# Performance work log

Measured on AMD Instinct MI355X. Metric: run time of the kernel, lower is better.

The kernel has to match this reference:

```python
import jax, jax.numpy as jnp
import numpy as np

N_LAYERS = 32
HIDDEN = 1024
INTER = 2816
BATCH = 256
INIT_SCALE = 0.02


def setup_inputs() -> dict:
    key = jax.random.key(0)
    k_h, k_g, k_u, k_d = jax.random.split(key, 4)
    down_std = INIT_SCALE / np.sqrt(2 * N_LAYERS)
    h = jax.random.normal(k_h, (BATCH, N_LAYERS, HIDDEN), dtype=jnp.float32)
    # torch Linear weight layout: (out_features, in_features); stack over experts
    Wg = jax.random.normal(k_g, (N_LAYERS, INTER, HIDDEN), dtype=jnp.float32) * INIT_SCALE
    Wu = jax.random.normal(k_u, (N_LAYERS, INTER, HIDDEN), dtype=jnp.float32) * INIT_SCALE
    Wd = jax.random.normal(k_d, (N_LAYERS, HIDDEN, INTER), dtype=jnp.float32) * down_std
    return {"h": h, "Wg": Wg, "Wu": Wu, "Wd": Wd}


def reference(h, Wg, Wu, Wd):
    # h: (B, N, D); Wg/Wu: (N, I, D); Wd: (N, D, I)
    gate = jnp.einsum("bnd,nid->bni", h, Wg)
    up = jnp.einsum("bnd,nid->bni", h, Wu)
    act = jax.nn.silu(gate) * up            # (B, N, I)
    out = jnp.einsum("bni,ndi->bnd", act, Wd)  # (B, N, D)
    return out
```

## Files before the change

kernel.cpp:

```cpp
#include <hip/hip_runtime.h>
#include <hip/hip_bf16.h>

#define BATCH   256
#define NLAYERS 32
#define HID     1024
#define INTER   2816
#define BK      64

typedef __attribute__((ext_vector_type(8))) short bf16x8;
typedef __attribute__((ext_vector_type(4))) float f32x4;
typedef __attribute__((ext_vector_type(4))) int   i32x4;

__device__ __forceinline__ ushort f2bf(float f) {
  union { float f; unsigned u; } v; v.f = f;
  unsigned u = v.u;
  u += 0x7FFFu + ((u >> 16) & 1u);
  return (ushort)(u >> 16);
}

__device__ __forceinline__ void cvt_store8(ushort* dst, f32x4 a, f32x4 b) {
  bf16x8 o;
  o[0] = (short)f2bf(a[0]); o[1] = (short)f2bf(a[1]);
  o[2] = (short)f2bf(a[2]); o[3] = (short)f2bf(a[3]);
  o[4] = (short)f2bf(b[0]); o[5] = (short)f2bf(b[1]);
  o[6] = (short)f2bf(b[2]); o[7] = (short)f2bf(b[3]);
  *(bf16x8*)dst = o;
}

__global__ __launch_bounds__(512) void k_gateup(
    const float* __restrict__ h, const float* __restrict__ Wg,
    const float* __restrict__ Wu, ushort* __restrict__ act) {
  const int bid   = blockIdx.x;
  const int layer = bid / (INTER / 64);
  const int itile = bid % (INTER / 64);
  const int i0    = itile * 64;
  const int tid   = threadIdx.x;
  const int lane  = tid & 63;
  const int wave  = tid >> 6;
  const int wm    = wave >> 1;
  const int wn    = wave & 1;

  __shared__ ushort lds[BATCH * BK + 2 * 64 * BK];
  ushort* Xl = lds;
  ushort* Gl = lds + BATCH * BK;
  ushort* Ul = Gl + 64 * BK;

  f32x4 ag[4][2] = {};
  f32x4 au[4][2] = {};

  int xrow[4], xkc[4], xldst[4];
  const float* xsrc[4];
#pragma unroll
  for (int r = 0; r < 4; ++r) {
    int g = tid + 512 * r;
    xrow[r] = g >> 3;
    xkc[r]  = g & 7;
    xldst[r] = xrow[r] * BK + ((xkc[r] ^ (xrow[r] & 7)) << 3);
    xsrc[r] = h + (size_t)xrow[r] * (NLAYERS * HID) + (size_t)layer * HID + xkc[r] * 8;
  }
  const int wrow = tid >> 3, wkc = tid & 7;
  const int wldst = wrow * BK + ((wkc ^ (wrow & 7)) << 3);
  const float* gsrc = Wg + (size_t)layer * INTER * HID + (size_t)(i0 + wrow) * HID + wkc * 8;
  const float* usrc = Wu + (size_t)layer * INTER * HID + (size_t)(i0 + wrow) * HID + wkc * 8;

  f32x4 rx[4][2], rg[2], ru[2];

#pragma unroll
  for (int r = 0; r < 4; ++r) { rx[r][0] = *(const f32x4*)xsrc[r]; rx[r][1] = *(const f32x4*)(xsrc[r] + 4); }
  rg[0] = *(const f32x4*)gsrc; rg[1] = *(const f32x4*)(gsrc + 4);
  ru[0] = *(const f32x4*)usrc; ru[1] = *(const f32x4*)(usrc + 4);

  const int NK = HID / BK;
  for (int k = 0; k < NK; ++k) {
    __syncthreads();
#pragma unroll
    for (int r = 0; r < 4; ++r) cvt_store8(&Xl[xldst[r]], rx[r][0], rx[r][1]);
    cvt_store8(&Gl[wldst], rg[0], rg[1]);
    cvt_store8(&Ul[wldst], ru[0], ru[1]);
    __syncthreads();

    if (k + 1 < NK) {
      int off = (k + 1) * BK;
#pragma unroll
      for (int r = 0; r < 4; ++r) {
        rx[r][0] = *(const f32x4*)(xsrc[r] + off);
        rx[r][1] = *(const f32x4*)(xsrc[r] + off + 4);
      }
      rg[0] = *(const f32x4*)(gsrc + off); rg[1] = *(const f32x4*)(gsrc + off + 4);
      ru[0] = *(const f32x4*)(usrc + off); ru[1] = *(const f32x4*)(usrc + off + 4);
    }

#pragma unroll
    for (int ks = 0; ks < 2; ++ks) {
      const int kg = ks * 4 + (lane >> 4);
      bf16x8 af[4];
#pragma unroll
      for (int m = 0; m < 4; ++m) {
        int row = wm * 64 + m * 16 + (lane & 15);
        af[m] = *(bf16x8*)&Xl[row * BK + ((kg ^ (row & 7)) << 3)];
      }
#pragma unroll
      for (int n = 0; n < 2; ++n) {
        int row = wn * 32 + n * 16 + (lane & 15);
        int u   = row * BK + ((kg ^ (row & 7)) << 3);
        bf16x8 bg = *(bf16x8*)&Gl[u];
        bf16x8 bu = *(bf16x8*)&Ul[u];
#pragma unroll
        for (int m = 0; m < 4; ++m) {
          ag[m][n] = __builtin_amdgcn_mfma_f32_16x16x32_bf16(af[m], bg, ag[m][n], 0, 0, 0);
          au[m][n] = __builtin_amdgcn_mfma_f32_16x16x32_bf16(af[m], bu, au[m][n], 0, 0, 0);
        }
      }
    }
  }

  const int c16 = lane & 15;
  const int r4  = (lane >> 4) * 4;
#pragma unroll
  for (int m = 0; m < 4; ++m)
#pragma unroll
    for (int n = 0; n < 2; ++n)
#pragma unroll
      for (int r = 0; r < 4; ++r) {
        float g = ag[m][n][r];
        float u = au[m][n][r];
        float a = (g / (1.f + __expf(-g))) * u;
        int b = wm * 64 + m * 16 + r4 + r;
        int i = i0 + wn * 32 + n * 16 + c16;
        act[((size_t)layer * BATCH + b) * INTER + i] = f2bf(a);
      }
}

__global__ __launch_bounds__(512) void k_down(
    const ushort* __restrict__ act, const float* __restrict__ Wd,
    float* __restrict__ out) {
  const int bid   = blockIdx.x;
  const int layer = bid / (HID / 64);
  const int dtile = bid % (HID / 64);
  const int d0    = dtile * 64;
  const int tid   = threadIdx.x;
  const int lane  = tid & 63;
  const int wave  = tid >> 6;
  const int wm    = wave >> 1;
  const int wn    = wave & 1;

  __shared__ ushort lds[BATCH * BK + 64 * BK];
  ushort* Al = lds;
  ushort* Wl = lds + BATCH * BK;

  f32x4 acc[4][2] = {};

  int arow[4], akc[4], aldst[4];
  const ushort* asrc[4];
#pragma unroll
  for (int r = 0; r < 4; ++r) {
    int g = tid + 512 * r;
    arow[r] = g >> 3;
    akc[r]  = g & 7;
    aldst[r] = arow[r] * BK + ((akc[r] ^ (arow[r] & 7)) << 3);
    asrc[r] = act + ((size_t)layer * BATCH + arow[r]) * INTER + akc[r] * 8;
  }
  const int wrow = tid >> 3, wkc = tid & 7;
  const int wldst = wrow * BK + ((wkc ^ (wrow & 7)) << 3);
  const float* wsrc = Wd + (size_t)layer * HID * INTER + (size_t)(d0 + wrow) * INTER + wkc * 8;

  i32x4 ra[4];
  f32x4 rw[2];

#pragma unroll
  for (int r = 0; r < 4; ++r) ra[r] = *(const i32x4*)asrc[r];
  rw[0] = *(const f32x4*)wsrc; rw[1] = *(const f32x4*)(wsrc + 4);

  const int NK = INTER / BK;
  for (int k = 0; k < NK; ++k) {
    __syncthreads();
#pragma unroll
    for (int r = 0; r < 4; ++r) *(i32x4*)&Al[aldst[r]] = ra[r];
    cvt_store8(&Wl[wldst], rw[0], rw[1]);
    __syncthreads();

    if (k + 1 < NK) {
      int off = (k + 1) * BK;
#pragma unroll
      for (int r = 0; r < 4; ++r) ra[r] = *(const i32x4*)(asrc[r] + off);
      rw[0] = *(const f32x4*)(wsrc + off); rw[1] = *(const f32x4*)(wsrc + off + 4);
    }

#pragma unroll
    for (int ks = 0; ks < 2; ++ks) {
      const int kg = ks * 4 + (lane >> 4);
      bf16x8 af[4];
#pragma unroll
      for (int m = 0; m < 4; ++m) {
        int row = wm * 64 + m * 16 + (lane & 15);
        af[m] = *(bf16x8*)&Al[row * BK + ((kg ^ (row & 7)) << 3)];
      }
#pragma unroll
      for (int n = 0; n < 2; ++n) {
        int row = wn * 32 + n * 16 + (lane & 15);
        bf16x8 bw = *(bf16x8*)&Wl[row * BK + ((kg ^ (row & 7)) << 3)];
#pragma unroll
        for (int m = 0; m < 4; ++m)
          acc[m][n] = __builtin_amdgcn_mfma_f32_16x16x32_bf16(af[m], bw, acc[m][n], 0, 0, 0);
      }
    }
  }

  const int c16 = lane & 15;
  const int r4  = (lane >> 4) * 4;
#pragma unroll
  for (int m = 0; m < 4; ++m)
#pragma unroll
    for (int n = 0; n < 2; ++n)
#pragma unroll
      for (int r = 0; r < 4; ++r) {
        int b = wm * 64 + m * 16 + r4 + r;
        int d = d0 + wn * 32 + n * 16 + c16;
        out[(size_t)b * (NLAYERS * HID) + (size_t)layer * HID + d] = acc[m][n][r];
      }
}

extern "C" void kernel_launch(void* const* d_in, const int* in_sizes, int n_in,
                              void* d_out, int out_size, void* d_ws, size_t ws_size,
                              hipStream_t stream) {
  const float* h  = (const float*)d_in[0];
  const float* Wg = (const float*)d_in[1];
  const float* Wu = (const float*)d_in[2];
  const float* Wd = (const float*)d_in[3];
  float* out  = (float*)d_out;
  ushort* act = (ushort*)d_ws;

  hipLaunchKernelGGL(k_gateup, dim3(NLAYERS * (INTER / 64)), dim3(512), 0, stream,
                     h, Wg, Wu, act);
  hipLaunchKernelGGL(k_down, dim3(NLAYERS * (HID / 64)), dim3(512), 0, stream,
                     act, Wd, out);
}
```

Measured before the change: 368.6 us.

## Retile gate/up kernel to 128x32 tiles with BK=32 and padded LDS

The gate/up kernel moves from 256-row by 64-column tiles with BK=64 and 512 threads to 128-row by 32-column tiles with BK=32 and 256 threads. It also replaces the XOR-swizzled LDS layout with a padded row stride and uses the library bf16 conversion when staging operands. This gives 4x more, smaller blocks and less LDS per block, which should raise occupancy and spread work across more CUs. In exchange, X and weight tiles are reused less, so each element of h and the weights is fetched more times, and the k loop takes twice as many barrier-separated steps.

Measured after the change: 439.6 us. 1.19x slower.

```diff
diff --git a/kernel.cpp b/kernel.cpp
--- a/kernel.cpp
+++ b/kernel.cpp
@@ -5,130 +5,130 @@
 #define NLAYERS 32
 #define HID     1024
 #define INTER   2816
-#define BK      64
 
 typedef __attribute__((ext_vector_type(8))) short bf16x8;
 typedef __attribute__((ext_vector_type(4))) float f32x4;
 typedef __attribute__((ext_vector_type(4))) int   i32x4;
 
 __device__ __forceinline__ ushort f2bf(float f) {
+  __hip_bfloat16 b = __float2bfloat16(f);
+  return *reinterpret_cast<ushort*>(&b);
+}
+
+__device__ __forceinline__ ushort f2bf_rne(float f) {
   union { float f; unsigned u; } v; v.f = f;
   unsigned u = v.u;
   u += 0x7FFFu + ((u >> 16) & 1u);
   return (ushort)(u >> 16);
 }
 
-__device__ __forceinline__ void cvt_store8(ushort* dst, f32x4 a, f32x4 b) {
-  bf16x8 o;
-  o[0] = (short)f2bf(a[0]); o[1] = (short)f2bf(a[1]);
-  o[2] = (short)f2bf(a[2]); o[3] = (short)f2bf(a[3]);
-  o[4] = (short)f2bf(b[0]); o[5] = (short)f2bf(b[1]);
-  o[6] = (short)f2bf(b[2]); o[7] = (short)f2bf(b[3]);
-  *(bf16x8*)dst = o;
-}
-
-__global__ __launch_bounds__(512) void k_gateup(
+__device__ __forceinline__ void cvt_store4(ushort* dst, f32x4 a) {
+  ushort4 o;
+  o.x = f2bf(a[0]); o.y = f2bf(a[1]); o.z = f2bf(a[2]); o.w = f2bf(a[3]);
+  *(ushort4*)dst = o;
+}
+
+#define LDR 40
+
+__global__ __launch_bounds__(256) void k_gateup(
     const float* __restrict__ h, const float* __restrict__ Wg,
     const float* __restrict__ Wu, ushort* __restrict__ act) {
   const int bid   = blockIdx.x;
-  const int layer = bid / (INTER / 64);
-  const int itile = bid % (INTER / 64);
-  const int i0    = itile * 64;
+  const int layer = bid / 176;
+  const int rem   = bid % 176;
+  const int it    = rem >> 1;
+  const int mt    = rem & 1;
+  const int i0    = it * 32;
+  const int m0    = mt * 128;
   const int tid   = threadIdx.x;
   const int lane  = tid & 63;
   const int wave  = tid >> 6;
   const int wm    = wave >> 1;
   const int wn    = wave & 1;
 
-  __shared__ ushort lds[BATCH * BK + 2 * 64 * BK];
-  ushort* Xl = lds;
-  ushort* Gl = lds + BATCH * BK;
-  ushort* Ul = Gl + 64 * BK;
-
-  f32x4 ag[4][2] = {};
-  f32x4 au[4][2] = {};
-
-  int xrow[4], xkc[4], xldst[4];
-  const float* xsrc[4];
+  __shared__ ushort Xl[128 * LDR];
+  __shared__ ushort Gl[32 * LDR];
+  __shared__ ushort Ul[32 * LDR];
+
+  f32x4 ag[4] = {}, au[4] = {};
+
+  const float* xsrc[4]; int xdst[4];
 #pragma unroll
   for (int r = 0; r < 4; ++r) {
-    int g = tid + 512 * r;
-    xrow[r] = g >> 3;
-    xkc[r]  = g & 7;
-    xldst[r] = xrow[r] * BK + ((xkc[r] ^ (xrow[r] & 7)) << 3);
-    xsrc[r] = h + (size_t)xrow[r] * (NLAYERS * HID) + (size_t)layer * HID + xkc[r] * 8;
-  }
-  const int wrow = tid >> 3, wkc = tid & 7;
-  const int wldst = wrow * BK + ((wkc ^ (wrow & 7)) << 3);
-  const float* gsrc = Wg + (size_t)layer * INTER * HID + (size_t)(i0 + wrow) * HID + wkc * 8;
-  const float* usrc = Wu + (size_t)layer * INTER * HID + (size_t)(i0 + wrow) * HID + wkc * 8;
-
-  f32x4 rx[4][2], rg[2], ru[2];
-
-#pragma unroll
-  for (int r = 0; r < 4; ++r) { rx[r][0] = *(const f32x4*)xsrc[r]; rx[r][1] = *(const f32x4*)(xsrc[r] + 4); }
-  rg[0] = *(const f32x4*)gsrc; rg[1] = *(const f32x4*)(gsrc + 4);
-  ru[0] = *(const f32x4*)usrc; ru[1] = *(const f32x4*)(usrc + 4);
-
-  const int NK = HID / BK;
+    int g = tid + 256 * r;
+    int row = g >> 3, u = g & 7;
+    xsrc[r] = h + (size_t)(m0 + row) * (NLAYERS * HID) + (size_t)layer * HID + u * 4;
+    xdst[r] = row * LDR + u * 4;
+  }
+  const int grow = tid >> 3, gu = tid & 7;
+  const int gdst = grow * LDR + gu * 4;
+  const float* gsrc = Wg + (size_t)layer * INTER * HID + (size_t)(i0 + grow) * HID + gu * 4;
+  const float* usrc = Wu + (size_t)layer * INTER * HID + (size_t)(i0 + grow) * HID + gu * 4;
+
+  f32x4 rx[4], rg, ru;
+#pragma unroll
+  for (int r = 0; r < 4; ++r) rx[r] = *(const f32x4*)xsrc[r];
+  rg = *(const f32x4*)gsrc;
+  ru = *(const f32x4*)usrc;
+
+  const int NK = HID / 32;
   for (int k = 0; k < NK; ++k) {
     __syncthreads();
 #pragma unroll
-    for (int r = 0; r < 4; ++r) cvt_store8(&Xl[xldst[r]], rx[r][0], rx[r][1]);
-    cvt_store8(&Gl[wldst], rg[0], rg[1]);
-    cvt_store8(&Ul[wldst], ru[0], ru[1]);
+    for (int r = 0; r < 4; ++r) cvt_store4(&Xl[xdst[r]], rx[r]);
+    cvt_store4(&Gl[gdst], rg);
+    cvt_store4(&Ul[gdst], ru);
     __syncthreads();
 
     if (k + 1 < NK) {
-      int off = (k + 1) * BK;
-#pragma unroll
-      for (int r = 0; r < 4; ++r) {
-        rx[r][0] = *(const f32x4*)(xsrc[r] + off);
-        rx[r][1] = *(const f32x4*)(xsrc[r] + off + 4);
-      }
-      rg[0] = *(const f32x4*)(gsrc + off); rg[1] = *(const f32x4*)(gsrc + off + 4);
-      ru[0] = *(const f32x4*)(usrc + off); ru[1] = *(const f32x4*)(usrc + off + 4);
-    }
-
-#pragma unroll
-    for (int ks = 0; ks < 2; ++ks) {
-      const int kg = ks * 4 + (lane >> 4);
-      bf16x8 af[4];
-#pragma unroll
-      for (int m = 0; m < 4; ++m) {
-        int row = wm * 64 + m * 16 + (lane & 15);
-        af[m] = *(bf16x8*)&Xl[row * BK + ((kg ^ (row & 7)) << 3)];
-      }
-#pragma unroll
-      for (int n = 0; n < 2; ++n) {
-        int row = wn * 32 + n * 16 + (lane & 15);
-        int u   = row * BK + ((kg ^ (row & 7)) << 3);
-        bf16x8 bg = *(bf16x8*)&Gl[u];
-        bf16x8 bu = *(bf16x8*)&Ul[u];
-#pragma unroll
-        for (int m = 0; m < 4; ++m) {
-          ag[m][n] = __builtin_amdgcn_mfma_f32_16x16x32_bf16(af[m], bg, ag[m][n], 0, 0, 0);
-          au[m][n] = __builtin_amdgcn_mfma_f32_16x16x32_bf16(af[m], bu, au[m][n], 0, 0, 0);
-        }
-      }
+      int off = (k + 1) * 32;
+#pragma unroll
+      for (int r = 0; r < 4; ++r) rx[r] = *(const f32x4*)(xsrc[r] + off);
+      rg = *(const f32x4*)(gsrc + off);
+      ru = *(const f32x4*)(usrc + off);
+    }
+
+    const int kg = lane >> 4;
+    bf16x8 af[4];
+#pragma unroll
+    for (int m = 0; m < 4; ++m) {
+      int row = wm * 64 + m * 16 + (lane & 15);
+      af[m] = *(bf16x8*)&Xl[row * LDR + kg * 8];
+    }
+    const int brow = wn * 16 + (lane & 15);
+    bf16x8 bg = *(bf16x8*)&Gl[brow * LDR + kg * 8];
+    bf16x8 bu = *(bf16x8*)&Ul[brow * LDR + kg * 8];
+#pragma unroll
+    for (int m = 0; m < 4; ++m) {
+      ag[m] = __builtin_amdgcn_mfma_f32_16x16x32_bf16(af[m], bg, ag[m], 0, 0, 0);
+      au[m] = __builtin_amdgcn_mfma_f32_16x16x32_bf16(af[m], bu, au[m], 0, 0, 0);
     }
   }
 
   const int c16 = lane & 15;
   const int r4  = (lane >> 4) * 4;
+  const int i   = i0 + wn * 16 + c16;
 #pragma unroll
   for (int m = 0; m < 4; ++m)
 #pragma unroll
-    for (int n = 0; n < 2; ++n)
-#pragma unroll
-      for (int r = 0; r < 4; ++r) {
-        float g = ag[m][n][r];
-        float u = au[m][n][r];
-        float a = (g / (1.f + __expf(-g))) * u;
-        int b = wm * 64 + m * 16 + r4 + r;
-        int i = i0 + wn * 32 + n * 16 + c16;
-        act[((size_t)layer * BATCH + b) * INTER + i] = f2bf(a);
-      }
+    for (int r = 0; r < 4; ++r) {
+      float g = ag[m][r];
+      float u = au[m][r];
+      float a = (g / (1.f + __expf(-g))) * u;
+      int b = m0 + wm * 64 + m * 16 + r4 + r;
+      act[((size_t)layer * BATCH + b) * INTER + i] = f2bf_rne(a);
+    }
+}
+
+#define BK 64
+
+__device__ __forceinline__ void cvt_store8(ushort* dst, f32x4 a, f32x4 b) {
+  bf16x8 o;
+  o[0] = (short)f2bf_rne(a[0]); o[1] = (short)f2bf_rne(a[1]);
+  o[2] = (short)f2bf_rne(a[2]); o[3] = (short)f2bf_rne(a[3]);
+  o[4] = (short)f2bf_rne(b[0]); o[5] = (short)f2bf_rne(b[1]);
+  o[6] = (short)f2bf_rne(b[2]); o[7] = (short)f2bf_rne(b[3]);
+  *(bf16x8*)dst = o;
 }
 
 __global__ __launch_bounds__(512) void k_down(
@@ -150,15 +150,14 @@
 
   f32x4 acc[4][2] = {};
 
-  int arow[4], akc[4], aldst[4];
+  int aldst[4];
   const ushort* asrc[4];
 #pragma unroll
   for (int r = 0; r < 4; ++r) {
     int g = tid + 512 * r;
-    arow[r] = g >> 3;
-    akc[r]  = g & 7;
-    aldst[r] = arow[r] * BK + ((akc[r] ^ (arow[r] & 7)) << 3);
-    asrc[r] = act + ((size_t)layer * BATCH + arow[r]) * INTER + akc[r] * 8;
+    int arow = g >> 3, akc = g & 7;
+    aldst[r] = arow * BK + ((akc ^ (arow & 7)) << 3);
+    asrc[r] = act + ((size_t)layer * BATCH + arow) * INTER + akc * 8;
   }
   const int wrow = tid >> 3, wkc = tid & 7;
   const int wldst = wrow * BK + ((wkc ^ (wrow & 7)) << 3);
@@ -230,7 +229,7 @@
   float* out  = (float*)d_out;
   ushort* act = (ushort*)d_ws;
 
-  hipLaunchKernelGGL(k_gateup, dim3(NLAYERS * (INTER / 64)), dim3(512), 0, stream,
+  hipLaunchKernelGGL(k_gateup, dim3(NLAYERS * 176), dim3(256), 0, stream,
                      h, Wg, Wu, act);
   hipLaunchKernelGGL(k_down, dim3(NLAYERS * (HID / 64)), dim3(512), 0, stream,
                      act, Wd, out);
```

## Restructure gate/up kernel: direct-register X loads, double-buffered weight LDS, smaller tiles

Applied to the files above, without the earlier changes.

The gate/up kernel now uses 32-wide intermediate tiles (twice as many blocks). Each wave loads its 32 batch rows of h straight from global memory into registers, converting them to bf16 fragments with no LDS staging. Gate and up weights go into a double-buffered LDS tile prefetched two steps ahead, leaving one barrier per k-step, and launch bounds request 4 blocks per CU. This trades fewer LDS bytes and barriers for more repeated global reads of h across blocks. It also swaps the hand-written bf16 rounding for the library conversion.

Result: slower. 513.7 us (+39.4%).

```diff
diff --git a/kernel.cpp b/kernel.cpp
--- a/kernel.cpp
+++ b/kernel.cpp
@@ -5,119 +5,117 @@
 #define NLAYERS 32
 #define HID     1024
 #define INTER   2816
-#define BK      64
 
 typedef __attribute__((ext_vector_type(8))) short bf16x8;
 typedef __attribute__((ext_vector_type(4))) float f32x4;
 typedef __attribute__((ext_vector_type(4))) int   i32x4;
 
 __device__ __forceinline__ ushort f2bf(float f) {
-  union { float f; unsigned u; } v; v.f = f;
-  unsigned u = v.u;
-  u += 0x7FFFu + ((u >> 16) & 1u);
-  return (ushort)(u >> 16);
-}
-
-__device__ __forceinline__ void cvt_store8(ushort* dst, f32x4 a, f32x4 b) {
+  __hip_bfloat16 b = __float2bfloat16(f);
+  return *reinterpret_cast<ushort*>(&b);
+}
+
+__device__ __forceinline__ bf16x8 cvt8(f32x4 a, f32x4 b) {
   bf16x8 o;
   o[0] = (short)f2bf(a[0]); o[1] = (short)f2bf(a[1]);
   o[2] = (short)f2bf(a[2]); o[3] = (short)f2bf(a[3]);
   o[4] = (short)f2bf(b[0]); o[5] = (short)f2bf(b[1]);
   o[6] = (short)f2bf(b[2]); o[7] = (short)f2bf(b[3]);
-  *(bf16x8*)dst = o;
-}
-
-__global__ __launch_bounds__(512) void k_gateup(
+  return o;
+}
+
+__global__ __launch_bounds__(512, 4) void k_gateup(
     const float* __restrict__ h, const float* __restrict__ Wg,
     const float* __restrict__ Wu, ushort* __restrict__ act) {
   const int bid   = blockIdx.x;
-  const int layer = bid / (INTER / 64);
-  const int itile = bid % (INTER / 64);
-  const int i0    = itile * 64;
+  const int layer = bid / (INTER / 32);
+  const int it    = bid % (INTER / 32);
+  const int i0    = it * 32;
   const int tid   = threadIdx.x;
   const int lane  = tid & 63;
   const int wave  = tid >> 6;
-  const int wm    = wave >> 1;
-  const int wn    = wave & 1;
-
-  __shared__ ushort lds[BATCH * BK + 2 * 64 * BK];
-  ushort* Xl = lds;
-  ushort* Gl = lds + BATCH * BK;
-  ushort* Ul = Gl + 64 * BK;
-
-  f32x4 ag[4][2] = {};
-  f32x4 au[4][2] = {};
-
-  int xrow[4], xkc[4], xldst[4];
-  const float* xsrc[4];
-#pragma unroll
-  for (int r = 0; r < 4; ++r) {
-    int g = tid + 512 * r;
-    xrow[r] = g >> 3;
-    xkc[r]  = g & 7;
-    xldst[r] = xrow[r] * BK + ((xkc[r] ^ (xrow[r] & 7)) << 3);
-    xsrc[r] = h + (size_t)xrow[r] * (NLAYERS * HID) + (size_t)layer * HID + xkc[r] * 8;
-  }
-  const int wrow = tid >> 3, wkc = tid & 7;
-  const int wldst = wrow * BK + ((wkc ^ (wrow & 7)) << 3);
-  const float* gsrc = Wg + (size_t)layer * INTER * HID + (size_t)(i0 + wrow) * HID + wkc * 8;
-  const float* usrc = Wu + (size_t)layer * INTER * HID + (size_t)(i0 + wrow) * HID + wkc * 8;
-
-  f32x4 rx[4][2], rg[2], ru[2];
-
-#pragma unroll
-  for (int r = 0; r < 4; ++r) { rx[r][0] = *(const f32x4*)xsrc[r]; rx[r][1] = *(const f32x4*)(xsrc[r] + 4); }
-  rg[0] = *(const f32x4*)gsrc; rg[1] = *(const f32x4*)(gsrc + 4);
-  ru[0] = *(const f32x4*)usrc; ru[1] = *(const f32x4*)(usrc + 4);
-
-  const int NK = HID / BK;
-  for (int k = 0; k < NK; ++k) {
+  const int m0    = wave * 32;
+
+  __shared__ ushort Wl[2][2][32 * 64];
+
+  f32x4 ag[2][2] = {}, au[2][2] = {};
+
+  const int half = tid >> 8;
+  const int w    = tid & 255;
+  const int wrow = w >> 3;
+  const int wsl  = w & 7;
+  const int wldst = wrow * 64 + ((wsl ^ (wrow & 7)) << 3);
+  const float* wsrc = (half ? Wu : Wg) +
+      (size_t)layer * INTER * HID + (size_t)(i0 + wrow) * HID + wsl * 8;
+
+  const int r16 = lane & 15;
+  const int g4  = lane >> 4;
+  const float* xp[2];
+#pragma unroll
+  for (int m = 0; m < 2; ++m)
+    xp[m] = h + (size_t)(m0 + m * 16 + r16) * (NLAYERS * HID) +
+            (size_t)layer * HID + g4 * 8;
+
+  f32x4 rw[2][2];
+  rw[0][0] = *(const f32x4*)(wsrc);       rw[0][1] = *(const f32x4*)(wsrc + 4);
+  rw[1][0] = *(const f32x4*)(wsrc + 64);  rw[1][1] = *(const f32x4*)(wsrc + 68);
+  *(bf16x8*)&Wl[0][half][wldst] = cvt8(rw[0][0], rw[0][1]);
+  __syncthreads();
+
+  const int NK = HID / 64;
+  for (int t = 0; t < NK; ++t) {
+    const int cur = t & 1;
+
+    if (t + 2 < NK) {
+      rw[t & 1][0] = *(const f32x4*)(wsrc + (t + 2) * 64);
+      rw[t & 1][1] = *(const f32x4*)(wsrc + (t + 2) * 64 + 4);
+    }
+    f32x4 xr[2][2][2];
+#pragma unroll
+    for (int ks = 0; ks < 2; ++ks)
+#pragma unroll
+      for (int m = 0; m < 2; ++m) {
+        const float* p = xp[m] + t * 64 + ks * 32;
+        xr[ks][m][0] = *(const f32x4*)p;
+        xr[ks][m][1] = *(const f32x4*)(p + 4);
+      }
+    if (t + 1 < NK)
+      *(bf16x8*)&Wl[cur ^ 1][half][wldst] = cvt8(rw[(t + 1) & 1][0], rw[(t + 1) & 1][1]);
+
+    bf16x8 xa[2][2];
+#pragma unroll
+    for (int ks = 0; ks < 2; ++ks)
+#pragma unroll
+      for (int m = 0; m < 2; ++m)
+        xa[ks][m] = cvt8(xr[ks][m][0], xr[ks][m][1]);
+
+#pragma unroll
+    for (int ks = 0; ks < 2; ++ks) {
+      const int kg = ks * 4 + g4;
+      bf16x8 bg[2], bu[2];
+#pragma unroll
+      for (int n = 0; n < 2; ++n) {
+        const int brow = n * 16 + r16;
+        const int u = brow * 64 + ((kg ^ (brow & 7)) << 3);
+        bg[n] = *(bf16x8*)&Wl[cur][0][u];
+        bu[n] = *(bf16x8*)&Wl[cur][1][u];
+      }
+#pragma unroll
+      for (int n = 0; n < 2; ++n)
+#pragma unroll
+        for (int m = 0; m < 2; ++m) {
+          ag[m][n] = __builtin_amdgcn_mfma_f32_16x16x32_bf16(xa[ks][m], bg[n], ag[m][n], 0, 0, 0);
+          au[m][n] = __builtin_amdgcn_mfma_f32_16x16x32_bf16(xa[ks][m], bu[n], au[m][n], 0, 0, 0);
+        }
+    }
+
     __syncthreads();
-#pragma unroll
-    for (int r = 0; r < 4; ++r) cvt_store8(&Xl[xldst[r]], rx[r][0], rx[r][1]);
-    cvt_store8(&Gl[wldst], rg[0], rg[1]);
-    cvt_store8(&Ul[wldst], ru[0], ru[1]);
-    __syncthreads();
-
-    if (k + 1 < NK) {
-      int off = (k + 1) * BK;
-#pragma unroll
-      for (int r = 0; r < 4; ++r) {
-        rx[r][0] = *(const f32x4*)(xsrc[r] + off);
-        rx[r][1] = *(const f32x4*)(xsrc[r] + off + 4);
-      }
-      rg[0] = *(const f32x4*)(gsrc + off); rg[1] = *(const f32x4*)(gsrc + off + 4);
-      ru[0] = *(const f32x4*)(usrc + off); ru[1] = *(const f32x4*)(usrc + off + 4);
-    }
-
-#pragma unroll
-    for (int ks = 0; ks < 2; ++ks) {
-      const int kg = ks * 4 + (lane >> 4);
-      bf16x8 af[4];
-#pragma unroll
-      for (int m = 0; m < 4; ++m) {
-        int row = wm * 64 + m * 16 + (lane & 15);
-        af[m] = *(bf16x8*)&Xl[row * BK + ((kg ^ (row & 7)) << 3)];
-      }
-#pragma unroll
-      for (int n = 0; n < 2; ++n) {
-        int row = wn * 32 + n * 16 + (lane & 15);
-        int u   = row * BK + ((kg ^ (row & 7)) << 3);
-        bf16x8 bg = *(bf16x8*)&Gl[u];
-        bf16x8 bu = *(bf16x8*)&Ul[u];
-#pragma unroll
-        for (int m = 0; m < 4; ++m) {
-          ag[m][n] = __builtin_amdgcn_mfma_f32_16x16x32_bf16(af[m], bg, ag[m][n], 0, 0, 0);
-          au[m][n] = __builtin_amdgcn_mfma_f32_16x16x32_bf16(af[m], bu, au[m][n], 0, 0, 0);
-        }
-      }
-    }
   }
 
   const int c16 = lane & 15;
   const int r4  = (lane >> 4) * 4;
 #pragma unroll
-  for (int m = 0; m < 4; ++m)
+  for (int m = 0; m < 2; ++m)
 #pragma unroll
     for (int n = 0; n < 2; ++n)
 #pragma unroll
@@ -125,10 +123,16 @@
         float g = ag[m][n][r];
         float u = au[m][n][r];
         float a = (g / (1.f + __expf(-g))) * u;
-        int b = wm * 64 + m * 16 + r4 + r;
-        int i = i0 + wn * 32 + n * 16 + c16;
+        int b = m0 + m * 16 + r4 + r;
+        int i = i0 + n * 16 + c16;
         act[((size_t)layer * BATCH + b) * INTER + i] = f2bf(a);
       }
+}
+
+#define BK 64
+
+__device__ __forceinline__ void cvt_store8(ushort* dst, f32x4 a, f32x4 b) {
+  *(bf16x8*)dst = cvt8(a, b);
 }
 
 __global__ __launch_bounds__(512) void k_down(
@@ -150,15 +154,14 @@
 
   f32x4 acc[4][2] = {};
 
-  int arow[4], akc[4], aldst[4];
+  int aldst[4];
   const ushort* asrc[4];
 #pragma unroll
   for (int r = 0; r < 4; ++r) {
     int g = tid + 512 * r;
-    arow[r] = g >> 3;
-    akc[r]  = g & 7;
-    aldst[r] = arow[r] * BK + ((akc[r] ^ (arow[r] & 7)) << 3);
-    asrc[r] = act + ((size_t)layer * BATCH + arow[r]) * INTER + akc[r] * 8;
+    int arow = g >> 3, akc = g & 7;
+    aldst[r] = arow * BK + ((akc ^ (arow & 7)) << 3);
+    asrc[r] = act + ((size_t)layer * BATCH + arow) * INTER + akc * 8;
   }
   const int wrow = tid >> 3, wkc = tid & 7;
   const int wldst = wrow * BK + ((wkc ^ (wrow & 7)) << 3);
@@ -230,7 +233,7 @@
   float* out  = (float*)d_out;
   ushort* act = (ushort*)d_ws;
 
-  hipLaunchKernelGGL(k_gateup, dim3(NLAYERS * (INTER / 64)), dim3(512), 0, stream,
+  hipLaunchKernelGGL(k_gateup, dim3(NLAYERS * (INTER / 32)), dim3(512), 0, stream,
                      h, Wg, Wu, act);
   hipLaunchKernelGGL(k_down, dim3(NLAYERS * (HID / 64)), dim3(512), 0, stream,
                      act, Wd, out);
```
